# Performance work log

Measured on AMD Instinct MI355X. Metric: run time of the kernel, lower is better.

## Reference

```python
import jax, jax.numpy as jnp
import numpy as np

B, H, W = 4, 128, 128
DIM, HEADS, WS, SS = 192, 6, 16, 8
CAT, NTOK, RD, DTD = 128, 64, 10, 64
MLPH, KSZ = 384, 5
LN_EPS = 1e-5


def _ln(x, g, b):
    mu = jnp.mean(x, axis=-1, keepdims=True)
    var = jnp.mean((x - mu) ** 2, axis=-1, keepdims=True)
    return (x - mu) * jax.lax.rsqrt(var + LN_EPS) * g + b


def _l2n(x):
    n = jnp.sqrt(jnp.sum(x * x, axis=-1, keepdims=True))
    return x / jnp.maximum(n, 1e-12)


def _win_part(x, ws):
    b, h, w, c = x.shape
    x = x.reshape(b, h // ws, ws, w // ws, ws, c).transpose(0, 1, 3, 2, 4, 5)
    return x.reshape(-1, ws, ws, c)


def _win_rev(win, ws, h, w):
    b = win.shape[0] // ((h // ws) * (w // ws))
    x = win.reshape(b, h // ws, w // ws, ws, ws, -1).transpose(0, 1, 3, 2, 4, 5)
    return x.reshape(b, h, w, -1)


def _make_rpi(ws):
    coords = np.stack(np.meshgrid(np.arange(ws), np.arange(ws), indexing='ij'))
    cf = coords.reshape(2, -1)
    rel = (cf[:, :, None] - cf[:, None, :]).transpose(1, 2, 0)
    rel[:, :, 0] += ws - 1
    rel[:, :, 1] += ws - 1
    rel[:, :, 0] *= 2 * ws - 1
    return rel.sum(-1)


def _make_attn_mask(h, w, ws, ss):
    img = np.zeros((1, h, w, 1), np.float32)
    cnt = 0
    for hs in (slice(0, -ws), slice(-ws, -ss), slice(-ss, None)):
        for vs in (slice(0, -ws), slice(-ws, -ss), slice(-ss, None)):
            img[:, hs, vs, :] = cnt
            cnt += 1
    mw = img.reshape(1, h // ws, ws, w // ws, ws, 1).transpose(0, 1, 3, 2, 4, 5).reshape(-1, ws * ws)
    am = mw[:, None, :] - mw[:, :, None]
    return np.where(am != 0, -100.0, 0.0).astype(np.float32)


def _fwd(x, td, attn_mask, rpi, h, w, norm1_g, norm1_b, norm2_g, norm2_b,
         wqkv_w, wqkv_b, wq_w, wq_b, wk_w, wk_b, wv_w, wv_b, atd_scale,
         aca_proj_w, aca_proj_b, rpb_table, win_proj_w, win_proj_b,
         fc_td_w, fc_td_b, fc1_w, fc1_b, dw_w, dw_b, fc2_w, fc2_b):
    b, n, c = x.shape
    shortcut = x
    xn = _ln(x, norm1_g, norm1_b)
    qkv = xn @ wqkv_w + wqkv_b  # (b, n, 3c)

    # --- ATD_CA: normalized cross-attention to token dictionary ---
    q = xn @ wq_w + wq_b          # (b, n, RD)
    k = td @ wk_w + wk_b          # (b, m, RD)
    v = td @ wv_w + wv_b          # (b, m, c)
    sim = jnp.einsum('bnr,bmr->bnm', _l2n(q), _l2n(k))
    scale = 1.0 + jnp.clip(atd_scale, 0.0, 3.0) * np.log(NTOK)
    sim = jax.nn.softmax(sim * scale, axis=-1)
    x_atd = sim @ v               # (b, n, c)

    # --- AC_MSA: category-sorted grouped attention ---
    tk_id = jnp.argmax(sim, axis=-1)                 # (b, n) int
    gs = min(n, CAT)
    ng = (n + gs - 1) // gs
    pad_n = ng * gs - n
    sidx = jnp.argsort(tk_id, axis=-1)
    inv = jnp.argsort(sidx, axis=-1)                 # inverse permutation
    sqkv = jnp.take_along_axis(qkv, sidx[:, :, None], axis=1)
    if pad_n > 0:
        sqkv = jnp.concatenate([sqkv, jnp.flip(sqkv[:, n - pad_n:n, :], axis=1)], axis=1)
    hd = c // HEADS
    g = sqkv.reshape(b, ng, gs, 3, HEADS, hd).transpose(3, 0, 1, 4, 2, 5)
    qg, kg, vg = g[0], g[1], g[2]
    ga = jax.nn.softmax(jnp.einsum('bghqd,bghkd->bghqk', qg, kg) * (hd ** -0.5), axis=-1)
    yg = jnp.einsum('bghqk,bghkd->bghqd', ga, vg).transpose(0, 1, 3, 2, 4).reshape(b, ng * gs, c)[:, :n]
    x_aca = jnp.take_along_axis(yg, inv[:, :, None], axis=1) @ aca_proj_w + aca_proj_b

    # --- per-token gathered token-dict features for the FFN ---
    td_f = td @ fc_td_w + fc_td_b                    # (b, m, DTD)
    x_td = jnp.take_along_axis(td_f, jnp.broadcast_to(tk_id[:, :, None], (b, n, DTD)), axis=1)

    # --- shifted window attention over qkv ---
    qkv_img = qkv.reshape(b, h, w, 3 * c)
    sh = jnp.roll(qkv_img, shift=(-SS, -SS), axis=(1, 2))
    xw = _win_part(sh, WS).reshape(-1, WS * WS, 3 * c)
    b_, nn_ = xw.shape[0], WS * WS
    wq3 = xw.reshape(b_, nn_, 3, HEADS, hd).transpose(2, 0, 3, 1, 4)
    qw, kw, vw = wq3[0] * (hd ** -0.5), wq3[1], wq3[2]
    aw = jnp.einsum('bhqd,bhkd->bhqk', qw, kw)
    rpb = rpb_table[rpi.reshape(-1)].reshape(nn_, nn_, HEADS).transpose(2, 0, 1)
    aw = aw + rpb[None]
    nw = attn_mask.shape[0]
    aw = (aw.reshape(b_ // nw, nw, HEADS, nn_, nn_) + attn_mask[None, :, None]).reshape(b_, HEADS, nn_, nn_)
    aw = jax.nn.softmax(aw, axis=-1)
    yw = jnp.einsum('bhqk,bhkd->bhqd', aw, vw).transpose(0, 2, 1, 3).reshape(b_, nn_, c)
    yw = yw @ win_proj_w + win_proj_b
    yw = _win_rev(yw.reshape(-1, WS, WS, c), WS, h, w)
    x_win = jnp.roll(yw, shift=(SS, SS), axis=(1, 2)).reshape(b, n, c)

    x = shortcut + x_win + x_atd + x_aca

    # --- ConvFFN with concatenated token-dict features + depthwise conv ---
    xn2 = _ln(x, norm2_g, norm2_b)
    x1 = jax.nn.gelu(xn2 @ fc1_w + fc1_b, approximate=False)
    xc = jnp.concatenate([x1, x_td], axis=-1)        # (b, n, MLPH+DTD)
    ch = MLPH + DTD
    img = xc.reshape(b, h, w, ch)
    cv = jax.lax.conv_general_dilated(img, dw_w, (1, 1), 'SAME',
                                      dimension_numbers=('NHWC', 'HWIO', 'NHWC'),
                                      feature_group_count=ch)
    cv = jax.nn.gelu(cv + dw_b, approximate=False).reshape(b, n, ch)
    x = x + (xc + cv) @ fc2_w + fc2_b
    return x


def setup_inputs():
    key = jax.random.key(0)
    ks = jax.random.split(key, 16)
    w02 = lambda k, s: jax.random.normal(k, s, jnp.float32) * 0.02
    return {
        'x': jax.random.normal(ks[0], (B, H * W, DIM), jnp.float32),
        'td': jax.random.normal(ks[1], (B, NTOK, DIM), jnp.float32),
        'attn_mask': jnp.asarray(_make_attn_mask(H, W, WS, SS)),
        'rpi': jnp.asarray(_make_rpi(WS), jnp.int32),
        'h': H, 'w': W,
        'norm1_g': jnp.ones((DIM,)), 'norm1_b': jnp.zeros((DIM,)),
        'norm2_g': jnp.ones((DIM,)), 'norm2_b': jnp.zeros((DIM,)),
        'wqkv_w': w02(ks[2], (DIM, 3 * DIM)), 'wqkv_b': jnp.zeros((3 * DIM,)),
        'wq_w': w02(ks[3], (DIM, RD)), 'wq_b': jnp.zeros((RD,)),
        'wk_w': w02(ks[4], (DIM, RD)), 'wk_b': jnp.zeros((RD,)),
        'wv_w': w02(ks[5], (DIM, DIM)), 'wv_b': jnp.zeros((DIM,)),
        'atd_scale': jnp.ones((1,)),
        'aca_proj_w': w02(ks[6], (DIM, DIM)), 'aca_proj_b': jnp.zeros((DIM,)),
        'rpb_table': w02(ks[7], ((2 * WS - 1) ** 2, HEADS)),
        'win_proj_w': w02(ks[8], (DIM, DIM)), 'win_proj_b': jnp.zeros((DIM,)),
        'fc_td_w': w02(ks[9], (DIM, DTD)), 'fc_td_b': jnp.zeros((DTD,)),
        'fc1_w': w02(ks[10], (DIM, MLPH)), 'fc1_b': jnp.zeros((MLPH,)),
        'dw_w': w02(ks[11], (KSZ, KSZ, 1, MLPH + DTD)), 'dw_b': jnp.zeros((MLPH + DTD,)),
        'fc2_w': w02(ks[12], (MLPH + DTD, DIM)), 'fc2_b': jnp.zeros((DIM,)),
    }


def reference(x, td, attn_mask, rpi, h, w, norm1_g, norm1_b, norm2_g, norm2_b,
              wqkv_w, wqkv_b, wq_w, wq_b, wk_w, wk_b, wv_w, wv_b, atd_scale,
              aca_proj_w, aca_proj_b, rpb_table, win_proj_w, win_proj_b,
              fc_td_w, fc_td_b, fc1_w, fc1_b, dw_w, dw_b, fc2_w, fc2_b):
    return _fwd(x, td, attn_mask, rpi, h, w, norm1_g, norm1_b, norm2_g, norm2_b,
                wqkv_w, wqkv_b, wq_w, wq_b, wk_w, wk_b, wv_w, wv_b, atd_scale,
                aca_proj_w, aca_proj_b, rpb_table, win_proj_w, win_proj_b,
                fc_td_w, fc_td_b, fc1_w, fc1_b, dw_w, dw_b, fc2_w, fc2_b)
```

## Files before the change

kernel.cpp:

```cpp
#include <hip/hip_runtime.h>
#include <hip/hip_bf16.h>
#include <math.h>

typedef __hip_bfloat16 bf16;
typedef short bf16x8 __attribute__((ext_vector_type(8)));
typedef float f32x4 __attribute__((ext_vector_type(4)));

#define NB 4
#define HH 128
#define WWID 128
#define CC 192
#define NPB (HH*WWID)
#define NT (NB*NPB)
#define NHEADS 6
#define HD 32
#define NTOK 64
#define RDIM 10
#define DTD 64
#define MLPH 384
#define CHF (MLPH+DTD)

__device__ __forceinline__ float b2f(bf16 v){ return __bfloat162float(v); }
__device__ __forceinline__ bf16  f2b(float v){ return __float2bfloat16(v); }
__device__ __forceinline__ float bfu(unsigned short u){ return __uint_as_float(((unsigned)u)<<16); }
__device__ __forceinline__ float geluf(float v){ return 0.5f*v*(1.0f+erff(v*0.70710678118654752f)); }
__device__ __forceinline__ int rg3(int v){ return v<112?0:(v<120?1:2); }

__device__ __forceinline__ void gload16(const void* g, void* l){
  __builtin_amdgcn_global_load_lds((const __attribute__((address_space(1))) unsigned*)g,
                                   (__attribute__((address_space(3))) unsigned*)l, 16, 0, 0);
}

__device__ __forceinline__ float wsumf(float v){
  #pragma unroll
  for (int m=32;m>0;m>>=1) v += __shfl_xor(v,m);
  return v;
}

__global__ void k_sentinel(float* out, int n, float v){
  int i = blockIdx.x*256+threadIdx.x;
  if (i<n) out[i]=v;
}

template<int BF16IN>
__global__ __launch_bounds__(256) void k_ln(const float* __restrict__ xf, const bf16* __restrict__ xb,
                                            const float* __restrict__ g, const float* __restrict__ be,
                                            bf16* __restrict__ out){
  int wave = threadIdx.x>>6, lane = threadIdx.x&63;
  int tok = blockIdx.x*4 + wave;
  size_t base = (size_t)tok*CC;
  float v0,v1,v2;
  if (BF16IN){ v0=b2f(xb[base+lane]); v1=b2f(xb[base+lane+64]); v2=b2f(xb[base+lane+128]); }
  else { v0=xf[base+lane]; v1=xf[base+lane+64]; v2=xf[base+lane+128]; }
  float s = wsumf(v0+v1+v2);
  float mu = s*(1.0f/192.0f);
  float d0=v0-mu, d1=v1-mu, d2=v2-mu;
  float q = wsumf(d0*d0+d1*d1+d2*d2);
  float rs = rsqrtf(q*(1.0f/192.0f)+1e-5f);
  out[base+lane]     = f2b(d0*rs*g[lane]     + be[lane]);
  out[base+lane+64]  = f2b(d1*rs*g[lane+64]  + be[lane+64]);
  out[base+lane+128] = f2b(d2*rs*g[lane+128] + be[lane+128]);
}

__global__ __launch_bounds__(256) void k_wt(const float* __restrict__ W, bf16* __restrict__ Wt, int K, int N){
  int i = blockIdx.x*256+threadIdx.x;
  if (i < K*N){ int n = i / K, k = i - n*K; Wt[i] = f2b(W[(size_t)k*N + n]); }
}

__global__ __launch_bounds__(256) void k_gw(const float* __restrict__ n1g, const float* __restrict__ n1b,
                                            const float* __restrict__ wq, const float* __restrict__ wqb,
                                            double* __restrict__ gw, double* __restrict__ S12){
  int ti=threadIdx.x;
  for (int i=ti;i<1920;i+=256){
    int c=i/10;
    gw[i]=(double)n1g[c]*(double)wq[i];
  }
  if (ti<10){
    double s1=0.0,s2=0.0;
    for (int c=0;c<192;c++){
      double w=(double)wq[c*10+ti];
      s1=fma((double)n1g[c],w,s1);
      s2=fma((double)n1b[c],w,s2);
    }
    S12[ti]=s1; S12[10+ti]=s2+(double)wqb[ti];
  }
}

__global__ __launch_bounds__(64) void k_kn(const float* __restrict__ td, const float* __restrict__ wk,
                                           const float* __restrict__ wkb, double* __restrict__ kn){
  int t = blockIdx.x*64+threadIdx.x;
  double kk[10]; double sq=0.0;
  const float* tr = td + (size_t)t*CC;
  #pragma unroll
  for (int r=0;r<10;r++) kk[r]=(double)wkb[r];
  for (int k=0;k<CC;k++){
    double tv=(double)tr[k];
    #pragma unroll
    for (int r=0;r<10;r++) kk[r] += tv*(double)wk[k*10+r];
  }
  #pragma unroll
  for (int r=0;r<10;r++) sq += kk[r]*kk[r];
  double inv = 1.0/fmax(sqrt(sq),1e-12);
  #pragma unroll
  for (int r=0;r<10;r++) kn[t*10+r]=kk[r]*inv;
}

__global__ __launch_bounds__(256) void k_v(const float* __restrict__ td, const float* __restrict__ wv,
                                           const float* __restrict__ wvb, float* __restrict__ vb){
  int idx = blockIdx.x*256+threadIdx.x;
  int c = idx % CC; int bm = idx / CC;
  const float* tr = td + (size_t)bm*CC;
  float a = wvb[c];
  for (int k=0;k<CC;k++) a = fmaf(tr[k], wv[(size_t)k*CC+c], a);
  vb[idx] = a;
}

__global__ __launch_bounds__(256) void k_tdf(const float* __restrict__ td, const float* __restrict__ w,
                                             const float* __restrict__ bb, float* __restrict__ tdf){
  int idx = blockIdx.x*256+threadIdx.x;
  int d = idx & 63; int bm = idx >> 6;
  const float* tr = td + (size_t)bm*CC;
  float a = bb[d];
  for (int k=0;k<CC;k++) a = fmaf(tr[k], w[(size_t)k*64+d], a);
  tdf[idx] = a;
}

__global__ __launch_bounds__(256) void k_rpbq(const int* __restrict__ rpi, const float* __restrict__ rpbt,
                                              bf16* __restrict__ rpbq){
  int idx = blockIdx.x*256+threadIdx.x;
  int h = idx>>16; int qk = idx&65535;
  rpbq[idx] = f2b(rpbt[rpi[qk]*6 + h]);
}

__global__ __launch_bounds__(256) void k_sim(const float* __restrict__ x, const double* __restrict__ gw,
                                             const double* __restrict__ S12, const double* __restrict__ kn,
                                             const float* __restrict__ atds,
                                             float* __restrict__ sim, int* __restrict__ tkid){
  __shared__ double gws[1920];
  __shared__ double S12s[20];
  __shared__ double ql[32][10];
  int ti = threadIdx.x;
  int blk = blockIdx.x;
  for (int i=ti;i<1920;i+=256) gws[i]=gw[i];
  if (ti<20) S12s[ti]=S12[ti];
  __syncthreads();
  {
    int tok = ti>>3, sub = ti&7;
    const float* xr = x + ((size_t)(blk*32+tok))*192 + sub*24;
    float xv[24];
    #pragma unroll
    for (int q4=0;q4<6;q4++) *(float4*)(xv+q4*4) = *(const float4*)(xr+q4*4);
    double acc[10]; double s=0.0, s2=0.0;
    #pragma unroll
    for (int r=0;r<10;r++) acc[r]=0.0;
    #pragma unroll
    for (int c=0;c<24;c++){
      double v=(double)xv[c];
      s+=v; s2=fma(v,v,s2);
      const double* gr = gws + (sub*24+c)*10;
      #pragma unroll
      for (int r=0;r<10;r++) acc[r]=fma(v,gr[r],acc[r]);
    }
    #pragma unroll
    for (int m=1;m<8;m<<=1){
      s+=__shfl_xor(s,m); s2+=__shfl_xor(s2,m);
      #pragma unroll
      for (int r=0;r<10;r++) acc[r]+=__shfl_xor(acc[r],m);
    }
    if (sub==0){
      double mu=s*(1.0/192.0);
      double var=s2*(1.0/192.0)-mu*mu;
      double rs=1.0/sqrt(var+1e-5);
      #pragma unroll
      for (int r=0;r<10;r++) ql[tok][r]=rs*(acc[r]-mu*S12s[r])+S12s[10+r];
    }
  }
  __syncthreads();
  int wave = ti>>6, lane = ti&63;
  int b = blk>>9;
  double kr[10];
  #pragma unroll
  for (int r2=0;r2<10;r2++) kr[r2]=kn[((size_t)(b*64+lane))*10+r2];
  double asd=fmin(fmax((double)atds[0],0.0),3.0);
  double scl=1.0+asd*4.1588830833596715;
  for (int tk=wave; tk<32; tk+=4){
    double dot=0.0, sq=0.0;
    #pragma unroll
    for (int r2=0;r2<10;r2++){
      double qv=ql[tk][r2];
      dot=fma(qv,kr[r2],dot);
      sq =fma(qv,qv,sq);
    }
    dot *= 1.0/fmax(sqrt(sq),1e-12);
    double bv=dot; int bi=lane;
    #pragma unroll
    for (int m2=32;m2>0;m2>>=1){
      double ov=__shfl_xor(bv,m2); int oi=__shfl_xor(bi,m2);
      if (ov>bv || (ov==bv && oi<bi)){ bv=ov; bi=oi; }
    }
    int tokg = blk*32+tk;
    if (lane==0) tkid[tokg]=bi;
    float t=(float)(dot*scl);
    float pp=__expf(t);
    float ssf=pp;
    #pragma unroll
    for (int m2=32;m2>0;m2>>=1) ssf+=__shfl_xor(ssf,m2);
    sim[(size_t)tokg*64+lane]=pp/ssf;
  }
}

template<int K, int KC, int NS, int ACT, int OUTMODE>
__global__ __launch_bounds__(256) void k_mm(const bf16* __restrict__ A, const bf16* __restrict__ Wt,
                                            const float* __restrict__ bias, const void* __restrict__ aux,
                                            void* __restrict__ outp){
  __shared__ __align__(16) char As[64*KC*2];
  __shared__ __align__(16) char Ws[64*KC*2];
  int row0 = blockIdx.x*64, n0 = blockIdx.y*64;
  int ti = threadIdx.x;
  int wave = ti>>6, lane = ti&63, g = lane>>4, l15 = lane&15;
  f32x4 acc[4];
  #pragma unroll
  for (int mt=0;mt<4;mt++){ f32x4 z={0.f,0.f,0.f,0.f}; acc[mt]=z; }
  const int KC8 = KC/8;
  for (int c0=0; c0<K; c0+=KC){
    if (c0) __syncthreads();
    if constexpr ((KC/8)%8==0){
      for (int u0 = wave*64; u0 < 64*KC8; u0 += 256){
        int u = u0 + lane;
        int r = u/KC8, kc = u - r*KC8;
        int kcs = kc ^ (r&7);
        gload16(A  + (size_t)(row0+r)*K + c0 + (kcs<<3), As + (size_t)u0*16);
        gload16(Wt + (size_t)(n0+r)*K  + c0 + (kcs<<3), Ws + (size_t)u0*16);
      }
    } else {
      for (int u=ti; u<64*KC8; u+=256){
        int r = u/KC8, kc = u-r*KC8;
        uint4 va = *(const uint4*)(A  + (size_t)(row0+r)*K + c0 + kc*8);
        *(uint4*)(As + ((r*(KC*2) + kc*16) ^ ((r&7)<<4))) = va;
        uint4 vw = *(const uint4*)(Wt + (size_t)(n0+r)*K + c0 + kc*8);
        *(uint4*)(Ws + ((r*(KC*2) + kc*16) ^ ((r&7)<<4))) = vw;
      }
    }
    __syncthreads();
    #pragma unroll
    for (int ks=0; ks<KC/32; ks++){
      int rw = wave*16 + l15;
      bf16x8 bfr = *(const bf16x8*)(Ws + ((rw*(KC*2) + ks*64 + g*16) ^ ((rw&7)<<4)));
      #pragma unroll
      for (int mt=0;mt<4;mt++){
        int ra = mt*16 + l15;
        bf16x8 af = *(const bf16x8*)(As + ((ra*(KC*2) + ks*64 + g*16) ^ ((ra&7)<<4)));
        acc[mt] = __builtin_amdgcn_mfma_f32_16x16x32_bf16(af, bfr, acc[mt], 0,0,0);
      }
    }
  }
  int col = n0 + wave*16 + l15;
  float bb = bias[col];
  #pragma unroll
  for (int mt=0;mt<4;mt++){
    #pragma unroll
    for (int j=0;j<4;j++){
      int row = row0 + mt*16 + g*4 + j;
      float v = acc[mt][j] + bb;
      if (OUTMODE==0){
        ((bf16*)outp)[(size_t)row*NS + col] = f2b(ACT ? geluf(v) : v);
      } else if (OUTMODE==2){
        size_t o = (size_t)row*NS + col;
        ((float*)outp)[o] = b2f(((const bf16*)aux)[o]) + v;
      } else if (OUTMODE==3){
        int win=row>>8, tii=row&255;
        int b=win>>6, wloc=win&63;
        int wy=wloc>>3, wx=wloc&7, tyy=tii>>4, txx=tii&15;
        int oy=(wy*16+tyy+8)&127, ox=(wx*16+txx+8)&127;
        size_t o=((size_t)(b*NPB + oy*128 + ox))*NS + col;
        ((bf16*)outp)[o] = f2b(((const float*)aux)[o] + v);
      } else {
        int orow=(row & ~(NPB-1)) + ((const int*)aux)[row];
        size_t o=(size_t)orow*NS + col;
        bf16* xo=(bf16*)outp;
        xo[o] = f2b(b2f(xo[o]) + v);
      }
    }
  }
}

__device__ __forceinline__ float ldw(const bf16* p, size_t i){ return __bfloat162float(p[i]); }
__device__ __forceinline__ float ldw(const float* p, size_t i){ return p[i]; }

template<int KD, int CB, typename WT>
__device__ __forceinline__ void gemm_core(const float (*As)[KD], const WT* __restrict__ W, int N, float (&acc)[8][CB]){
  int tid = threadIdx.x;
  for (int k=0;k<KD;k+=4){
    float w0[CB],w1[CB],w2[CB],w3[CB];
    #pragma unroll
    for (int j=0;j<CB;j++){
      int c = tid + 64*j;
      w0[j]=ldw(W,(size_t)(k+0)*N+c);
      w1[j]=ldw(W,(size_t)(k+1)*N+c);
      w2[j]=ldw(W,(size_t)(k+2)*N+c);
      w3[j]=ldw(W,(size_t)(k+3)*N+c);
    }
    #pragma unroll
    for (int r=0;r<8;r++){
      float4 a = *reinterpret_cast<const float4*>(&As[r][k]);
      #pragma unroll
      for (int j=0;j<CB;j++)
        acc[r][j]=fmaf(a.x,w0[j],fmaf(a.y,w1[j],fmaf(a.z,w2[j],fmaf(a.w,w3[j],acc[r][j]))));
    }
  }
}

__global__ __launch_bounds__(64) void k_xatd(const float* __restrict__ sim, const float* __restrict__ vb,
                                             bf16* __restrict__ xacc){
  __shared__ __align__(16) float As[8][64];
  int row0=blockIdx.x*8;
  for (int idx=threadIdx.x; idx<8*64; idx+=64){
    int r=idx>>6, k=idx&63;
    As[r][k]=sim[(size_t)(row0+r)*64+k];
  }
  __syncthreads();
  float acc[8][3]={};
  const float* Wv = vb + (size_t)(row0>>14)*64*CC;
  gemm_core<64,3>(As, Wv, CC, acc);
  int tid=threadIdx.x;
  #pragma unroll
  for (int j=0;j<3;j++){
    int c=tid+64*j;
    #pragma unroll
    for (int r=0;r<8;r++){
      size_t o=(size_t)(row0+r)*CC+c;
      xacc[o]=f2b(b2f(xacc[o])+acc[r][j]);
    }
  }
}

__global__ __launch_bounds__(256) void k_tdgather(const float* __restrict__ tdf, const int* __restrict__ tkid,
                                                  bf16* __restrict__ xc){
  int idx = blockIdx.x*256+threadIdx.x;
  int d = idx & 63; int tok = idx >> 6;
  int b = tok >> 14;
  int m = tkid[tok];
  xc[(size_t)tok*CHF + MLPH + d] = f2b(tdf[((size_t)((b<<6)+m))*64 + d]);
}

__global__ __launch_bounds__(256) void k_hist(const int* __restrict__ tkid, int* __restrict__ chist){
  __shared__ int h[64];
  int b = blockIdx.x>>6, ch = blockIdx.x&63;
  if (threadIdx.x<64) h[threadIdx.x]=0;
  __syncthreads();
  int v = tkid[b*NPB + ch*256 + threadIdx.x];
  atomicAdd(&h[v],1);
  __syncthreads();
  if (threadIdx.x<64) chist[(size_t)blockIdx.x*64 + threadIdx.x] = h[threadIdx.x];
}

__global__ __launch_bounds__(64) void k_scan(const int* __restrict__ chist, int* __restrict__ coff,
                                             int* __restrict__ bstart){
  int b = blockIdx.x; int v = threadIdx.x;
  __shared__ int tot[64], bs[64];
  int s=0;
  for (int ch=0; ch<64; ch++){
    coff[((size_t)(b*64+ch))*64+v] = s;
    s += chist[((size_t)(b*64+ch))*64+v];
  }
  tot[v]=s;
  __syncthreads();
  if (v==0){ int run=0; for (int u=0;u<64;u++){ bs[u]=run; run+=tot[u]; } }
  __syncthreads();
  bstart[b*64+v] = bs[v];
}

__global__ __launch_bounds__(256) void k_place(const int* __restrict__ tkid, const int* __restrict__ coff,
                                               const int* __restrict__ bstart, int* __restrict__ sidx){
  __shared__ int vals[256];
  int b = blockIdx.x>>6, ch = blockIdx.x&63;
  int tid = threadIdx.x;
  int tok = ch*256 + tid;
  int v = tkid[b*NPB + tok];
  vals[tid]=v;
  __syncthreads();
  int lr=0;
  for (int j=0;j<tid;j++) lr += (vals[j]==v);
  int pos = bstart[b*64+v] + coff[((size_t)(b*64+ch))*64+v] + lr;
  sidx[b*NPB + pos] = tok;
}

__global__ __launch_bounds__(256,4) void k_acattn(const bf16* __restrict__ qkv, const int* __restrict__ sidx,
                                                  bf16* __restrict__ yg){
  __shared__ bf16 Kl[128*32];
  __shared__ bf16 Vt[32*128];
  __shared__ bf16 Ps[4][16*32];
  int bid=blockIdx.x;
  int h = bid % NHEADS; int gg = (bid/NHEADS) & 127; int b = bid/(NHEADS*128);
  int ti = threadIdx.x;
  if (ti < 128){
    int srow = b*NPB + sidx[b*NPB + gg*128 + ti];
    const bf16* src = qkv + (size_t)srow*576 + 192 + h*32;
    const uint4* s4 = (const uint4*)src;
    char* kb = (char*)Kl;
    #pragma unroll
    for (int w=0;w<4;w++) *(uint4*)(kb + ((ti*64 + w*16) ^ ((ti&7)<<4))) = s4[w];
    const bf16* vsrc = src + 192;
    char* vbp = (char*)Vt;
    #pragma unroll
    for (int d=0;d<32;d++) *(bf16*)(vbp + ((d*256 + ti*2) ^ ((d&7)<<4))) = vsrc[d];
  }
  __syncthreads();
  int wave=ti>>6, lane=ti&63, g=lane>>4, l15=lane&15;
  bf16x8 qf[2];
  #pragma unroll
  for (int qt=0;qt<2;qt++){
    int q = wave*32 + qt*16 + l15;
    int srow = b*NPB + sidx[b*NPB + gg*128 + q];
    qf[qt] = *(const bf16x8*)(qkv + (size_t)srow*576 + h*32 + g*8);
  }
  f32x4 O[2][2]; float lsp[2][4];
  #pragma unroll
  for (int qt=0;qt<2;qt++){
    #pragma unroll
    for (int dt=0;dt<2;dt++){ f32x4 z={0.f,0.f,0.f,0.f}; O[qt][dt]=z; }
    #pragma unroll
    for (int j=0;j<4;j++) lsp[qt][j]=0.f;
  }
  const float rsc=0.17677669529663687f;
  const char* kb=(const char*)Kl; const char* vbp=(const char*)Vt;
  for (int st=0; st<4; st++){
    int r0=st*32+l15, r1=st*32+16+l15;
    bf16x8 kf0 = *(const bf16x8*)(kb + ((r0*64 + g*16) ^ ((r0&7)<<4)));
    bf16x8 kf1 = *(const bf16x8*)(kb + ((r1*64 + g*16) ^ ((r1&7)<<4)));
    int d0=l15, d1=16+l15;
    bf16x8 vf0 = *(const bf16x8*)(vbp + ((d0*256 + st*64 + g*16) ^ ((d0&7)<<4)));
    bf16x8 vf1 = *(const bf16x8*)(vbp + ((d1*256 + st*64 + g*16) ^ ((d1&7)<<4)));
    #pragma unroll
    for (int qt=0;qt<2;qt++){
      f32x4 z={0.f,0.f,0.f,0.f};
      f32x4 s0 = __builtin_amdgcn_mfma_f32_16x16x32_bf16(qf[qt], kf0, z, 0,0,0);
      f32x4 s1 = __builtin_amdgcn_mfma_f32_16x16x32_bf16(qf[qt], kf1, z, 0,0,0);
      float p0[4],p1[4];
      char* pb=(char*)Ps[wave];
      #pragma unroll
      for (int j=0;j<4;j++){
        p0[j]=__expf(fminf(s0[j]*rsc,80.f));
        p1[j]=__expf(fminf(s1[j]*rsc,80.f));
        lsp[qt][j]+=p0[j]+p1[j];
        int q=g*4+j;
        *(bf16*)(pb + ((q*64 + l15*2) ^ ((q&7)<<4)))      = f2b(p0[j]);
        *(bf16*)(pb + ((q*64 + 32 + l15*2) ^ ((q&7)<<4))) = f2b(p1[j]);
      }
      bf16x8 pa = *(const bf16x8*)((const char*)Ps[wave] + ((l15*64 + g*16) ^ ((l15&7)<<4)));
      O[qt][0]=__builtin_amdgcn_mfma_f32_16x16x32_bf16(pa, vf0, O[qt][0], 0,0,0);
      O[qt][1]=__builtin_amdgcn_mfma_f32_16x16x32_bf16(pa, vf1, O[qt][1], 0,0,0);
    }
  }
  #pragma unroll
  for (int qt=0;qt<2;qt++){
    #pragma unroll
    for (int msk=1; msk<16; msk<<=1){
      #pragma unroll
      for (int j=0;j<4;j++) lsp[qt][j]+=__shfl_xor(lsp[qt][j],msk);
    }
    #pragma unroll
    for (int j=0;j<4;j++){
      float inv=1.0f/lsp[qt][j];
      int q = wave*32 + qt*16 + g*4 + j;
      bf16* yo = yg + ((size_t)(b*NPB + gg*128 + q))*CC + h*32;
      yo[l15]    = f2b(O[qt][0][j]*inv);
      yo[16+l15] = f2b(O[qt][1][j]*inv);
    }
  }
}

__global__ __launch_bounds__(256,3) void k_winattn(const bf16* __restrict__ qkv, const bf16* __restrict__ rpbq,
                                                   bf16* __restrict__ yw){
  __shared__ bf16 Kl[256*32];
  __shared__ bf16 Vt[32*256];
  __shared__ bf16 Ps[4][16*32];
  int bid = blockIdx.x;
  int h = bid % NHEADS; int win = bid / NHEADS;
  int b = win >> 6; int wloc = win & 63;
  int wy = wloc >> 3, wx = wloc & 7;
  int ti = threadIdx.x;
  {
    int ty=ti>>4, tx=ti&15;
    int oy=(wy*16+ty+8)&127, ox=(wx*16+tx+8)&127;
    const bf16* src = qkv + (size_t)(b*NPB+oy*128+ox)*576 + 192 + h*32;
    const uint4* s4 = (const uint4*)src;
    char* kb = (char*)Kl;
    #pragma unroll
    for (int w=0;w<4;w++) *(uint4*)(kb + ((ti*64 + w*16) ^ ((ti&7)<<4))) = s4[w];
    const bf16* vsrc = src + 192;
    char* vbp = (char*)Vt;
    #pragma unroll
    for (int d=0;d<32;d++) *(bf16*)(vbp + ((d*512 + ti*2) ^ ((d&7)<<4))) = vsrc[d];
  }
  __syncthreads();
  int wave=ti>>6, lane=ti&63, g=lane>>4, l15=lane&15;
  bf16x8 qf[4];
  #pragma unroll
  for (int qt=0;qt<4;qt++){
    int ty=wave*4+qt, tx=l15;
    int oy=(wy*16+ty+8)&127, ox=(wx*16+tx+8)&127;
    qf[qt] = *(const bf16x8*)(qkv + (size_t)(b*NPB+oy*128+ox)*576 + h*32 + g*8);
  }
  f32x4 O[4][2]; float lsp[4][4];
  #pragma unroll
  for (int qt=0;qt<4;qt++){
    #pragma unroll
    for (int dt=0;dt<2;dt++){ f32x4 z={0.f,0.f,0.f,0.f}; O[qt][dt]=z; }
    #pragma unroll
    for (int j=0;j<4;j++) lsp[qt][j]=0.f;
  }
  const float rsc=0.17677669529663687f;
  int rxk = rg3(wx*16+l15);
  int rxq[4], ryq[4];
  #pragma unroll
  for (int j=0;j<4;j++) rxq[j]=rg3(wx*16+g*4+j);
  #pragma unroll
  for (int qt=0;qt<4;qt++) ryq[qt]=rg3(wy*16+wave*4+qt);
  const char* kb=(const char*)Kl; const char* vbp=(const char*)Vt;
  for (int st=0; st<8; st++){
    int r0=st*32+l15, r1=st*32+16+l15;
    bf16x8 kf0 = *(const bf16x8*)(kb + ((r0*64 + g*16) ^ ((r0&7)<<4)));
    bf16x8 kf1 = *(const bf16x8*)(kb + ((r1*64 + g*16) ^ ((r1&7)<<4)));
    int d0=l15, d1=16+l15;
    bf16x8 vf0 = *(const bf16x8*)(vbp + ((d0*512 + st*64 + g*16) ^ ((d0&7)<<4)));
    bf16x8 vf1 = *(const bf16x8*)(vbp + ((d1*512 + st*64 + g*16) ^ ((d1&7)<<4)));
    int rk0 = rg3(wy*16+st*2)*3   + rxk;
    int rk1 = rg3(wy*16+st*2+1)*3 + rxk;
    #pragma unroll
    for (int qt=0;qt<4;qt++){
      f32x4 z={0.f,0.f,0.f,0.f};
      f32x4 s0 = __builtin_amdgcn_mfma_f32_16x16x32_bf16(qf[qt], kf0, z, 0,0,0);
      f32x4 s1 = __builtin_amdgcn_mfma_f32_16x16x32_bf16(qf[qt], kf1, z, 0,0,0);
      int qr0 = wave*64 + qt*16 + g*4;
      float p0[4],p1[4];
      char* pb=(char*)Ps[wave];
      #pragma unroll
      for (int j=0;j<4;j++){
        const bf16* rb = rpbq + (((size_t)h*256 + qr0 + j)<<8) + st*32;
        int rq = ryq[qt]*3 + rxq[j];
        float b0 = b2f(rb[l15])    + (rq!=rk0 ? -100.f : 0.f);
        float b1 = b2f(rb[16+l15]) + (rq!=rk1 ? -100.f : 0.f);
        p0[j]=__expf(fminf(fmaf(s0[j],rsc,b0),80.f));
        p1[j]=__expf(fminf(fmaf(s1[j],rsc,b1),80.f));
        lsp[qt][j]+=p0[j]+p1[j];
        int q=g*4+j;
        *(bf16*)(pb + ((q*64 + l15*2) ^ ((q&7)<<4)))      = f2b(p0[j]);
        *(bf16*)(pb + ((q*64 + 32 + l15*2) ^ ((q&7)<<4))) = f2b(p1[j]);
      }
      bf16x8 pa = *(const bf16x8*)((const char*)Ps[wave] + ((l15*64 + g*16) ^ ((l15&7)<<4)));
      O[qt][0]=__builtin_amdgcn_mfma_f32_16x16x32_bf16(pa, vf0, O[qt][0], 0,0,0);
      O[qt][1]=__builtin_amdgcn_mfma_f32_16x16x32_bf16(pa, vf1, O[qt][1], 0,0,0);
    }
  }
  #pragma unroll
  for (int qt=0;qt<4;qt++){
    #pragma unroll
    for (int msk=1; msk<16; msk<<=1){
      #pragma unroll
      for (int j=0;j<4;j++) lsp[qt][j]+=__shfl_xor(lsp[qt][j],msk);
    }
    #pragma unroll
    for (int j=0;j<4;j++){
      float inv=1.0f/lsp[qt][j];
      int q = wave*64 + qt*16 + g*4 + j;
      bf16* yo = yw + ((size_t)win*256 + q)*CC + h*32;
      yo[l15]    = f2b(O[qt][0][j]*inv);
      yo[16+l15] = f2b(O[qt][1][j]*inv);
    }
  }
}

__global__ __launch_bounds__(256,4) void k_dw(const bf16* __restrict__ xc, const float* __restrict__ dww,
                                              const float* __restrict__ dwb, bf16* __restrict__ sv){
  int tid = blockIdx.x*256 + threadIdx.x;
  int ch8 = tid % 56; int pt = tid / 56;
  int x0 = (pt & 31)*4; int yq = (pt>>5)&127; int b = pt>>12;
  float acc[4][8];
  #pragma unroll
  for (int p=0;p<4;p++)
    #pragma unroll
    for (int c=0;c<8;c++) acc[p][c]=0.f;
  unsigned choff = (unsigned)ch8*8;
  const float* wp = dww + choff;
  #pragma unroll
  for (int dy=0;dy<5;dy++){
    int yy = yq+dy-2;
    if ((unsigned)yy>127u) continue;
    float4 w0[5], w1[5];
    #pragma unroll
    for (int dx=0;dx<5;dx++){
      w0[dx] = *(const float4*)(wp + (dy*5+dx)*CHF);
      w1[dx] = *(const float4*)(wp + (dy*5+dx)*CHF + 4);
    }
    unsigned rowoff = ((unsigned)(b<<14) + ((unsigned)yy<<7))*CHF + choff;
    #pragma unroll
    for (int j=0;j<8;j++){
      int ox = x0-2+j;
      if ((unsigned)ox>127u) continue;
      uint4 v = *(const uint4*)(xc + rowoff + (unsigned)ox*CHF);
      float u[8];
      unsigned vv[4]={v.x,v.y,v.z,v.w};
      #pragma unroll
      for (int t=0;t<4;t++){
        u[2*t]  = __uint_as_float(vv[t]<<16);
        u[2*t+1]= __uint_as_float(vv[t]&0xffff0000u);
      }
      #pragma unroll
      for (int dx=0;dx<5;dx++){
        int p = j-dx;
        if (p<0 || p>3) continue;
        acc[p][0]=fmaf(u[0],w0[dx].x,acc[p][0]);
        acc[p][1]=fmaf(u[1],w0[dx].y,acc[p][1]);
        acc[p][2]=fmaf(u[2],w0[dx].z,acc[p][2]);
        acc[p][3]=fmaf(u[3],w0[dx].w,acc[p][3]);
        acc[p][4]=fmaf(u[4],w1[dx].x,acc[p][4]);
        acc[p][5]=fmaf(u[5],w1[dx].y,acc[p][5]);
        acc[p][6]=fmaf(u[6],w1[dx].z,acc[p][6]);
        acc[p][7]=fmaf(u[7],w1[dx].w,acc[p][7]);
      }
    }
  }
  float4 b0 = *(const float4*)(dwb + choff);
  float4 b1 = *(const float4*)(dwb + choff + 4);
  float bb[8]={b0.x,b0.y,b0.z,b0.w,b1.x,b1.y,b1.z,b1.w};
  unsigned obase = ((unsigned)(b<<14) + ((unsigned)yq<<7) + (unsigned)x0)*CHF + choff;
  #pragma unroll
  for (int p=0;p<4;p++){
    uint4 cv4 = *(const uint4*)(xc + obase + (unsigned)p*CHF);
    unsigned vv[4]={cv4.x,cv4.y,cv4.z,cv4.w};
    bf16 o[8];
    #pragma unroll
    for (int t=0;t<4;t++){
      float c0 = __uint_as_float(vv[t]<<16);
      float c1 = __uint_as_float(vv[t]&0xffff0000u);
      o[2*t]   = f2b(c0 + geluf(acc[p][2*t]  + bb[2*t]));
      o[2*t+1] = f2b(c1 + geluf(acc[p][2*t+1]+ bb[2*t+1]));
    }
    *(uint4*)(sv + obase + (unsigned)p*CHF) = *(const uint4*)o;
  }
}

extern "C" void kernel_launch(void* const* d_in, const int* in_sizes, int n_in,
                              void* d_out, int out_size, void* d_ws, size_t ws_size,
                              hipStream_t stream){
  const float* x    = (const float*)d_in[0];
  const float* td   = (const float*)d_in[1];
  const int*   rpi  = (const int*)d_in[3];
  const float* n1g  = (const float*)d_in[6];
  const float* n1b  = (const float*)d_in[7];
  const float* n2g  = (const float*)d_in[8];
  const float* n2b  = (const float*)d_in[9];
  const float* wqkv = (const float*)d_in[10];
  const float* wqkvb= (const float*)d_in[11];
  const float* wq   = (const float*)d_in[12];
  const float* wqb  = (const float*)d_in[13];
  const float* wk   = (const float*)d_in[14];
  const float* wkb  = (const float*)d_in[15];
  const float* wv   = (const float*)d_in[16];
  const float* wvb  = (const float*)d_in[17];
  const float* atds = (const float*)d_in[18];
  const float* acaw = (const float*)d_in[19];
  const float* acab = (const float*)d_in[20];
  const float* rpbt = (const float*)d_in[21];
  const float* winw = (const float*)d_in[22];
  const float* winb = (const float*)d_in[23];
  const float* tdw  = (const float*)d_in[24];
  const float* tdbb = (const float*)d_in[25];
  const float* f1w  = (const float*)d_in[26];
  const float* f1b  = (const float*)d_in[27];
  const float* dww  = (const float*)d_in[28];
  const float* dwb  = (const float*)d_in[29];
  const float* f2w  = (const float*)d_in[30];
  const float* f2bb = (const float*)d_in[31];
  float* out = (float*)d_out;

  const size_t QKV_BYTES = (size_t)NT*576*2;
  const size_t XN_BYTES  = (size_t)NT*CC*2;
  const size_t XC_BYTES  = (size_t)NT*CHF*2;

  char* base = (char*)d_ws;
  size_t off = 0;
  auto give = [&](size_t bytes)->char*{
    off = (off + 255) & ~(size_t)255;
    char* r = base + off; off += bytes; return r;
  };
  char*   qkv_r = give(QKV_BYTES);
  char*   xn_r  = give(XN_BYTES);
  char*   sim_r = give(XN_BYTES);
  bf16*   xacc  = (bf16*)  give(XN_BYTES);
  int*    tkid  = (int*)   give((size_t)NT*4);
  int*    sidx  = (int*)   give((size_t)NT*4);
  double* kn    = (double*)give((size_t)NB*64*RDIM*8);
  float*  vbuf  = (float*) give((size_t)NB*64*CC*4);
  float*  tdf   = (float*) give((size_t)NB*64*DTD*4);
  int*    chist = (int*)   give((size_t)NB*64*64*4);
  int*    coff  = (int*)   give((size_t)NB*64*64*4);
  int*    bstart= (int*)   give((size_t)NB*64*4);
  bf16*   rpbq  = (bf16*)  give((size_t)NHEADS*256*256*2);
  bf16*   wqkvt = (bf16*)  give((size_t)192*576*2);
  bf16*   f1wt  = (bf16*)  give((size_t)192*384*2);
  bf16*   f2wt  = (bf16*)  give((size_t)448*192*2);
  bf16*   winwt = (bf16*)  give((size_t)192*192*2);
  bf16*   acawt = (bf16*)  give((size_t)192*192*2);
  double* gw    = (double*)give((size_t)1920*8);
  double* S12   = (double*)give((size_t)20*8);

  if (off > ws_size){
    k_sentinel<<<(out_size+255)/256,256,0,stream>>>(out, out_size, (float)(ws_size>>20));
    return;
  }

  bf16*  qkv  = (bf16*)qkv_r;
  bf16*  xc   = (bf16*)qkv_r;
  bf16*  sv   = (bf16*)(qkv_r + XC_BYTES);
  bf16*  xn   = (bf16*)xn_r;
  bf16*  atmp = (bf16*)xn_r;
  float* sim  = (float*)sim_r;

  k_wt<<<(192*576+255)/256,256,0,stream>>>(wqkv, wqkvt, 192, 576);
  k_wt<<<(192*384+255)/256,256,0,stream>>>(f1w, f1wt, 192, 384);
  k_wt<<<(448*192+255)/256,256,0,stream>>>(f2w, f2wt, 448, 192);
  k_wt<<<(192*192+255)/256,256,0,stream>>>(winw, winwt, 192, 192);
  k_wt<<<(192*192+255)/256,256,0,stream>>>(acaw, acawt, 192, 192);
  k_gw<<<1,256,0,stream>>>(n1g, n1b, wq, wqb, gw, S12);
  k_ln<0><<<NT/4,256,0,stream>>>(x, nullptr, n1g, n1b, xn);
  k_mm<192,192,576,0,0><<<dim3(NT/64,9),256,0,stream>>>(xn, wqkvt, wqkvb, nullptr, qkv);
  k_rpbq<<<NHEADS*256*256/256,256,0,stream>>>(rpi, rpbt, rpbq);
  k_winattn<<<NB*64*NHEADS,256,0,stream>>>(qkv, rpbq, atmp);
  k_mm<192,192,192,0,3><<<dim3(NT/64,3),256,0,stream>>>(atmp, winwt, winb, x, xacc);
  k_kn<<<4,64,0,stream>>>(td, wk, wkb, kn);
  k_v<<<(NB*64*CC)/256,256,0,stream>>>(td, wv, wvb, vbuf);
  k_tdf<<<(NB*64*DTD)/256,256,0,stream>>>(td, tdw, tdbb, tdf);
  k_sim<<<NT/32,256,0,stream>>>(x, gw, S12, kn, atds, sim, tkid);
  k_hist<<<NB*64,256,0,stream>>>(tkid, chist);
  k_scan<<<NB,64,0,stream>>>(chist, coff, bstart);
  k_place<<<NB*64,256,0,stream>>>(tkid, coff, bstart, sidx);
  k_acattn<<<NB*128*NHEADS,256,0,stream>>>(qkv, sidx, atmp);
  k_mm<192,192,192,0,4><<<dim3(NT/64,3),256,0,stream>>>(atmp, acawt, acab, sidx, xacc);
  k_xatd<<<NT/8,64,0,stream>>>(sim, vbuf, xacc);
  k_tdgather<<<NT*64/256,256,0,stream>>>(tdf, tkid, xc);
  k_ln<1><<<NT/4,256,0,stream>>>(nullptr, xacc, n2g, n2b, xn);
  k_mm<192,192,448,1,0><<<dim3(NT/64,6),256,0,stream>>>(xn, f1wt, f1b, nullptr, xc);
  k_dw<<<NT*56/4/256,256,0,stream>>>(xc, dww, dwb, sv);
  k_mm<448,64,192,0,2><<<dim3(NT/64,3),256,0,stream>>>(sv, f2wt, f2bb, xacc, out);
}
```

Measured before the change: 540.1 us.

## Fuse LayerNorm into GEMM prologue for qkv and fc1 projections

Removes the standalone LayerNorm kernels and instead normalizes input rows inside the GEMM kernel while staging the A tile into shared memory. This avoids writing and re-reading the normalized bf16 activation buffer. In exchange, each column-block of the GEMM recomputes the normalization and re-reads the raw fp32/bf16 input. Variance is also now computed with a single-pass sum of squares.

New measurement: 592.4 us. 1.1x slower.

```diff
diff --git a/kernel.cpp b/kernel.cpp
--- a/kernel.cpp
+++ b/kernel.cpp
@@ -42,26 +42,6 @@
   if (i<n) out[i]=v;
 }
 
-template<int BF16IN>
-__global__ __launch_bounds__(256) void k_ln(const float* __restrict__ xf, const bf16* __restrict__ xb,
-                                            const float* __restrict__ g, const float* __restrict__ be,
-                                            bf16* __restrict__ out){
-  int wave = threadIdx.x>>6, lane = threadIdx.x&63;
-  int tok = blockIdx.x*4 + wave;
-  size_t base = (size_t)tok*CC;
-  float v0,v1,v2;
-  if (BF16IN){ v0=b2f(xb[base+lane]); v1=b2f(xb[base+lane+64]); v2=b2f(xb[base+lane+128]); }
-  else { v0=xf[base+lane]; v1=xf[base+lane+64]; v2=xf[base+lane+128]; }
-  float s = wsumf(v0+v1+v2);
-  float mu = s*(1.0f/192.0f);
-  float d0=v0-mu, d1=v1-mu, d2=v2-mu;
-  float q = wsumf(d0*d0+d1*d1+d2*d2);
-  float rs = rsqrtf(q*(1.0f/192.0f)+1e-5f);
-  out[base+lane]     = f2b(d0*rs*g[lane]     + be[lane]);
-  out[base+lane+64]  = f2b(d1*rs*g[lane+64]  + be[lane+64]);
-  out[base+lane+128] = f2b(d2*rs*g[lane+128] + be[lane+128]);
-}
-
 __global__ __launch_bounds__(256) void k_wt(const float* __restrict__ W, bf16* __restrict__ Wt, int K, int N){
   int i = blockIdx.x*256+threadIdx.x;
   if (i < K*N){ int n = i / K, k = i - n*K; Wt[i] = f2b(W[(size_t)k*N + n]); }
@@ -209,10 +189,12 @@
   }
 }
 
-template<int K, int KC, int NS, int ACT, int OUTMODE>
+template<int K, int KC, int NS, int ACT, int OUTMODE, int LNIN>
 __global__ __launch_bounds__(256) void k_mm(const bf16* __restrict__ A, const bf16* __restrict__ Wt,
                                             const float* __restrict__ bias, const void* __restrict__ aux,
-                                            void* __restrict__ outp){
+                                            void* __restrict__ outp,
+                                            const void* __restrict__ lnx, const float* __restrict__ lng,
+                                            const float* __restrict__ lnb){
   __shared__ __align__(16) char As[64*KC*2];
   __shared__ __align__(16) char Ws[64*KC*2];
   int row0 = blockIdx.x*64, n0 = blockIdx.y*64;
@@ -224,7 +206,51 @@
   const int KC8 = KC/8;
   for (int c0=0; c0<K; c0+=KC){
     if (c0) __syncthreads();
-    if constexpr ((KC/8)%8==0){
+    if constexpr (LNIN != 0){
+      static_assert(K==192 && KC==192, "LNIN requires K=KC=192");
+      int r = ti>>2, q4 = ti&3;
+      float xv[48];
+      if constexpr (LNIN==1){
+        const float* xr = (const float*)lnx + (size_t)(row0+r)*192 + q4*48;
+        #pragma unroll
+        for (int i=0;i<12;i++) *(float4*)(xv+i*4) = *(const float4*)(xr+i*4);
+      } else {
+        const bf16* xr = (const bf16*)lnx + (size_t)(row0+r)*192 + q4*48;
+        #pragma unroll
+        for (int i=0;i<6;i++){
+          bf16x8 v8 = *(const bf16x8*)(xr+i*8);
+          #pragma unroll
+          for (int c=0;c<8;c++) xv[i*8+c]=bfu((unsigned short)v8[c]);
+        }
+      }
+      float s=0.f, s2=0.f;
+      #pragma unroll
+      for (int c=0;c<48;c++){ s+=xv[c]; s2=fmaf(xv[c],xv[c],s2); }
+      s  += __shfl_xor(s,1);  s2 += __shfl_xor(s2,1);
+      s  += __shfl_xor(s,2);  s2 += __shfl_xor(s2,2);
+      float mu = s*(1.0f/192.0f);
+      float var = s2*(1.0f/192.0f) - mu*mu;
+      float rs = rsqrtf(var+1e-5f);
+      #pragma unroll
+      for (int i=0;i<6;i++){
+        int ch0 = q4*48 + i*8;
+        float4 g0 = *(const float4*)(lng+ch0), g1 = *(const float4*)(lng+ch0+4);
+        float4 b0 = *(const float4*)(lnb+ch0), b1 = *(const float4*)(lnb+ch0+4);
+        float gg[8]={g0.x,g0.y,g0.z,g0.w,g1.x,g1.y,g1.z,g1.w};
+        float bbv[8]={b0.x,b0.y,b0.z,b0.w,b1.x,b1.y,b1.z,b1.w};
+        bf16 tmp[8];
+        #pragma unroll
+        for (int c=0;c<8;c++) tmp[c]=f2b((xv[i*8+c]-mu)*rs*gg[c]+bbv[c]);
+        int kc = q4*6 + i;
+        *(uint4*)(As + ((r*(KC*2) + kc*16) ^ ((r&7)<<4))) = *(const uint4*)tmp;
+      }
+      for (int u0 = wave*64; u0 < 64*KC8; u0 += 256){
+        int u = u0 + lane;
+        int rr = u/KC8, kc = u - rr*KC8;
+        int kcs = kc ^ (rr&7);
+        gload16(Wt + (size_t)(n0+rr)*K + (kcs<<3), Ws + (size_t)u0*16);
+      }
+    } else if constexpr ((KC/8)%8==0){
       for (int u0 = wave*64; u0 < 64*KC8; u0 += 256){
         int u = u0 + lane;
         int r = u/KC8, kc = u - r*KC8;
@@ -714,7 +740,6 @@
   bf16*  qkv  = (bf16*)qkv_r;
   bf16*  xc   = (bf16*)qkv_r;
   bf16*  sv   = (bf16*)(qkv_r + XC_BYTES);
-  bf16*  xn   = (bf16*)xn_r;
   bf16*  atmp = (bf16*)xn_r;
   float* sim  = (float*)sim_r;
 
@@ -724,11 +749,10 @@
   k_wt<<<(192*192+255)/256,256,0,stream>>>(winw, winwt, 192, 192);
   k_wt<<<(192*192+255)/256,256,0,stream>>>(acaw, acawt, 192, 192);
   k_gw<<<1,256,0,stream>>>(n1g, n1b, wq, wqb, gw, S12);
-  k_ln<0><<<NT/4,256,0,stream>>>(x, nullptr, n1g, n1b, xn);
-  k_mm<192,192,576,0,0><<<dim3(NT/64,9),256,0,stream>>>(xn, wqkvt, wqkvb, nullptr, qkv);
+  k_mm<192,192,576,0,0,1><<<dim3(NT/64,9),256,0,stream>>>(nullptr, wqkvt, wqkvb, nullptr, qkv, x, n1g, n1b);
   k_rpbq<<<NHEADS*256*256/256,256,0,stream>>>(rpi, rpbt, rpbq);
   k_winattn<<<NB*64*NHEADS,256,0,stream>>>(qkv, rpbq, atmp);
-  k_mm<192,192,192,0,3><<<dim3(NT/64,3),256,0,stream>>>(atmp, winwt, winb, x, xacc);
+  k_mm<192,192,192,0,3,0><<<dim3(NT/64,3),256,0,stream>>>(atmp, winwt, winb, x, xacc, nullptr, nullptr, nullptr);
   k_kn<<<4,64,0,stream>>>(td, wk, wkb, kn);
   k_v<<<(NB*64*CC)/256,256,0,stream>>>(td, wv, wvb, vbuf);
   k_tdf<<<(NB*64*DTD)/256,256,0,stream>>>(td, tdw, tdbb, tdf);
@@ -737,11 +761,10 @@
   k_scan<<<NB,64,0,stream>>>(chist, coff, bstart);
   k_place<<<NB*64,256,0,stream>>>(tkid, coff, bstart, sidx);
   k_acattn<<<NB*128*NHEADS,256,0,stream>>>(qkv, sidx, atmp);
-  k_mm<192,192,192,0,4><<<dim3(NT/64,3),256,0,stream>>>(atmp, acawt, acab, sidx, xacc);
+  k_mm<192,192,192,0,4,0><<<dim3(NT/64,3),256,0,stream>>>(atmp, acawt, acab, sidx, xacc, nullptr, nullptr, nullptr);
   k_xatd<<<NT/8,64,0,stream>>>(sim, vbuf, xacc);
   k_tdgather<<<NT*64/256,256,0,stream>>>(tdf, tkid, xc);
-  k_ln<1><<<NT/4,256,0,stream>>>(nullptr, xacc, n2g, n2b, xn);
-  k_mm<192,192,448,1,0><<<dim3(NT/64,6),256,0,stream>>>(xn, f1wt, f1b, nullptr, xc);
+  k_mm<192,192,448,1,0,2><<<dim3(NT/64,6),256,0,stream>>>(nullptr, f1wt, f1b, nullptr, xc, xacc, n2g, n2b);
   k_dw<<<NT*56/4/256,256,0,stream>>>(xc, dww, dwb, sv);
-  k_mm<448,64,192,0,2><<<dim3(NT/64,3),256,0,stream>>>(sv, f2wt, f2bb, xacc, out);
-}
+  k_mm<448,64,192,0,2,0><<<dim3(NT/64,3),256,0,stream>>>(sv, f2wt, f2bb, xacc, out, nullptr, nullptr, nullptr);
+}
```

## Compute three 64-column output tiles per GEMM block to reuse A tile

Applied to the files above, without the earlier changes.

The GEMM kernel now has each block loop over three 64-wide column tiles. The A tile stays resident in shared memory while the weight tile is reloaded for each column tile, and the grid's y dimension shrinks by a factor of three. This cuts global reads of the activation matrix and the number of blocks launched. In exchange it uses more accumulator registers, adds barriers, serializes weight loads against compute, and leaves fewer blocks to fill the GPU.

New measurement: 541.9 us. Within noise of the previous version (+0.3%).

```diff
diff --git a/kernel.cpp b/kernel.cpp
--- a/kernel.cpp
+++ b/kernel.cpp
@@ -209,76 +209,84 @@
   }
 }
 
-template<int K, int KC, int NS, int ACT, int OUTMODE>
+template<int K, int KC, int NS, int NTILE, int ACT, int OUTMODE>
 __global__ __launch_bounds__(256) void k_mm(const bf16* __restrict__ A, const bf16* __restrict__ Wt,
                                             const float* __restrict__ bias, const void* __restrict__ aux,
                                             void* __restrict__ outp){
+  static_assert((KC/8)%8==0, "async staging requires KC8 multiple of 8");
   __shared__ __align__(16) char As[64*KC*2];
   __shared__ __align__(16) char Ws[64*KC*2];
-  int row0 = blockIdx.x*64, n0 = blockIdx.y*64;
+  int row0 = blockIdx.x*64, ncol0 = blockIdx.y*(64*NTILE);
   int ti = threadIdx.x;
   int wave = ti>>6, lane = ti&63, g = lane>>4, l15 = lane&15;
-  f32x4 acc[4];
-  #pragma unroll
-  for (int mt=0;mt<4;mt++){ f32x4 z={0.f,0.f,0.f,0.f}; acc[mt]=z; }
+  f32x4 acc[NTILE][4];
+  #pragma unroll
+  for (int nt=0;nt<NTILE;nt++)
+    #pragma unroll
+    for (int mt=0;mt<4;mt++){ f32x4 z={0.f,0.f,0.f,0.f}; acc[nt][mt]=z; }
   const int KC8 = KC/8;
   for (int c0=0; c0<K; c0+=KC){
     if (c0) __syncthreads();
-    if constexpr ((KC/8)%8==0){
-      for (int u0 = wave*64; u0 < 64*KC8; u0 += 256){
-        int u = u0 + lane;
-        int r = u/KC8, kc = u - r*KC8;
-        int kcs = kc ^ (r&7);
-        gload16(A  + (size_t)(row0+r)*K + c0 + (kcs<<3), As + (size_t)u0*16);
-        gload16(Wt + (size_t)(n0+r)*K  + c0 + (kcs<<3), Ws + (size_t)u0*16);
+    for (int u0 = wave*64; u0 < 64*KC8; u0 += 256){
+      int u = u0 + lane;
+      int r = u/KC8, kc = u - r*KC8;
+      int kcs = kc ^ (r&7);
+      gload16(A  + (size_t)(row0+r)*K  + c0 + (kcs<<3), As + (size_t)u0*16);
+      gload16(Wt + (size_t)(ncol0+r)*K + c0 + (kcs<<3), Ws + (size_t)u0*16);
+    }
+    #pragma unroll
+    for (int nt=0; nt<NTILE; nt++){
+      __syncthreads();
+      #pragma unroll
+      for (int ks=0; ks<KC/32; ks++){
+        int rw = wave*16 + l15;
+        bf16x8 bfr = *(const bf16x8*)(Ws + ((rw*(KC*2) + ks*64 + g*16) ^ ((rw&7)<<4)));
+        #pragma unroll
+        for (int mt=0;mt<4;mt++){
+          int ra = mt*16 + l15;
+          bf16x8 af = *(const bf16x8*)(As + ((ra*(KC*2) + ks*64 + g*16) ^ ((ra&7)<<4)));
+          acc[nt][mt] = __builtin_amdgcn_mfma_f32_16x16x32_bf16(af, bfr, acc[nt][mt], 0,0,0);
+        }
       }
-    } else {
-      for (int u=ti; u<64*KC8; u+=256){
-        int r = u/KC8, kc = u-r*KC8;
-        uint4 va = *(const uint4*)(A  + (size_t)(row0+r)*K + c0 + kc*8);
-        *(uint4*)(As + ((r*(KC*2) + kc*16) ^ ((r&7)<<4))) = va;
-        uint4 vw = *(const uint4*)(Wt + (size_t)(n0+r)*K + c0 + kc*8);
-        *(uint4*)(Ws + ((r*(KC*2) + kc*16) ^ ((r&7)<<4))) = vw;
+      if (nt+1 < NTILE){
+        __syncthreads();
+        for (int u0 = wave*64; u0 < 64*KC8; u0 += 256){
+          int u = u0 + lane;
+          int r = u/KC8, kc = u - r*KC8;
+          int kcs = kc ^ (r&7);
+          gload16(Wt + (size_t)(ncol0+(nt+1)*64+r)*K + c0 + (kcs<<3), Ws + (size_t)u0*16);
+        }
       }
     }
-    __syncthreads();
-    #pragma unroll
-    for (int ks=0; ks<KC/32; ks++){
-      int rw = wave*16 + l15;
-      bf16x8 bfr = *(const bf16x8*)(Ws + ((rw*(KC*2) + ks*64 + g*16) ^ ((rw&7)<<4)));
-      #pragma unroll
-      for (int mt=0;mt<4;mt++){
-        int ra = mt*16 + l15;
-        bf16x8 af = *(const bf16x8*)(As + ((ra*(KC*2) + ks*64 + g*16) ^ ((ra&7)<<4)));
-        acc[mt] = __builtin_amdgcn_mfma_f32_16x16x32_bf16(af, bfr, acc[mt], 0,0,0);
-      }
-    }
-  }
-  int col = n0 + wave*16 + l15;
-  float bb = bias[col];
-  #pragma unroll
-  for (int mt=0;mt<4;mt++){
-    #pragma unroll
-    for (int j=0;j<4;j++){
-      int row = row0 + mt*16 + g*4 + j;
-      float v = acc[mt][j] + bb;
-      if (OUTMODE==0){
-        ((bf16*)outp)[(size_t)row*NS + col] = f2b(ACT ? geluf(v) : v);
-      } else if (OUTMODE==2){
-        size_t o = (size_t)row*NS + col;
-        ((float*)outp)[o] = b2f(((const bf16*)aux)[o]) + v;
-      } else if (OUTMODE==3){
-        int win=row>>8, tii=row&255;
-        int b=win>>6, wloc=win&63;
-        int wy=wloc>>3, wx=wloc&7, tyy=tii>>4, txx=tii&15;
-        int oy=(wy*16+tyy+8)&127, ox=(wx*16+txx+8)&127;
-        size_t o=((size_t)(b*NPB + oy*128 + ox))*NS + col;
-        ((bf16*)outp)[o] = f2b(((const float*)aux)[o] + v);
-      } else {
-        int orow=(row & ~(NPB-1)) + ((const int*)aux)[row];
-        size_t o=(size_t)orow*NS + col;
-        bf16* xo=(bf16*)outp;
-        xo[o] = f2b(b2f(xo[o]) + v);
+  }
+  #pragma unroll
+  for (int nt=0; nt<NTILE; nt++){
+    int col = ncol0 + nt*64 + wave*16 + l15;
+    float bb = bias[col];
+    #pragma unroll
+    for (int mt=0;mt<4;mt++){
+      #pragma unroll
+      for (int j=0;j<4;j++){
+        int row = row0 + mt*16 + g*4 + j;
+        float v = acc[nt][mt][j] + bb;
+        if (OUTMODE==0){
+          ((bf16*)outp)[(size_t)row*NS + col] = f2b(ACT ? geluf(v) : v);
+        } else if (OUTMODE==2){
+          size_t o = (size_t)row*NS + col;
+          ((float*)outp)[o] = b2f(((const bf16*)aux)[o]) + v;
+        } else if (OUTMODE==3){
+          int win=row>>8, tii=row&255;
+          int b=win>>6, wloc=win&63;
+          int wy=wloc>>3, wx=wloc&7, tyy=tii>>4, txx=tii&15;
+          int oy=(wy*16+tyy+8)&127, ox=(wx*16+txx+8)&127;
+          size_t o=((size_t)(b*NPB + oy*128 + ox))*NS + col;
+          ((bf16*)outp)[o] = f2b(((const float*)aux)[o] + v);
+        } else {
+          int orow=(row & ~(NPB-1)) + ((const int*)aux)[row];
+          size_t o=(size_t)orow*NS + col;
+          bf16* xo=(bf16*)outp;
+          xo[o] = f2b(b2f(xo[o]) + v);
+        }
       }
     }
   }
@@ -725,10 +733,10 @@
   k_wt<<<(192*192+255)/256,256,0,stream>>>(acaw, acawt, 192, 192);
   k_gw<<<1,256,0,stream>>>(n1g, n1b, wq, wqb, gw, S12);
   k_ln<0><<<NT/4,256,0,stream>>>(x, nullptr, n1g, n1b, xn);
-  k_mm<192,192,576,0,0><<<dim3(NT/64,9),256,0,stream>>>(xn, wqkvt, wqkvb, nullptr, qkv);
+  k_mm<192,192,576,3,0,0><<<dim3(NT/64,3),256,0,stream>>>(xn, wqkvt, wqkvb, nullptr, qkv);
   k_rpbq<<<NHEADS*256*256/256,256,0,stream>>>(rpi, rpbt, rpbq);
   k_winattn<<<NB*64*NHEADS,256,0,stream>>>(qkv, rpbq, atmp);
-  k_mm<192,192,192,0,3><<<dim3(NT/64,3),256,0,stream>>>(atmp, winwt, winb, x, xacc);
+  k_mm<192,192,192,3,0,3><<<dim3(NT/64,1),256,0,stream>>>(atmp, winwt, winb, x, xacc);
   k_kn<<<4,64,0,stream>>>(td, wk, wkb, kn);
   k_v<<<(NB*64*CC)/256,256,0,stream>>>(td, wv, wvb, vbuf);
   k_tdf<<<(NB*64*DTD)/256,256,0,stream>>>(td, tdw, tdbb, tdf);
@@ -737,11 +745,11 @@
   k_scan<<<NB,64,0,stream>>>(chist, coff, bstart);
   k_place<<<NB*64,256,0,stream>>>(tkid, coff, bstart, sidx);
   k_acattn<<<NB*128*NHEADS,256,0,stream>>>(qkv, sidx, atmp);
-  k_mm<192,192,192,0,4><<<dim3(NT/64,3),256,0,stream>>>(atmp, acawt, acab, sidx, xacc);
+  k_mm<192,192,192,3,0,4><<<dim3(NT/64,1),256,0,stream>>>(atmp, acawt, acab, sidx, xacc);
   k_xatd<<<NT/8,64,0,stream>>>(sim, vbuf, xacc);
   k_tdgather<<<NT*64/256,256,0,stream>>>(tdf, tkid, xc);
   k_ln<1><<<NT/4,256,0,stream>>>(nullptr, xacc, n2g, n2b, xn);
-  k_mm<192,192,448,1,0><<<dim3(NT/64,6),256,0,stream>>>(xn, f1wt, f1b, nullptr, xc);
+  k_mm<192,192,448,3,1,0><<<dim3(NT/64,2),256,0,stream>>>(xn, f1wt, f1b, nullptr, xc);
   k_dw<<<NT*56/4/256,256,0,stream>>>(xc, dww, dwb, sv);
-  k_mm<448,64,192,0,2><<<dim3(NT/64,3),256,0,stream>>>(sv, f2wt, f2bb, xacc, out);
-}
+  k_mm<448,64,192,3,0,2><<<dim3(NT/64,1),256,0,stream>>>(sv, f2wt, f2bb, xacc, out);
+}
```
